# Kernel optimization log

Hardware: AMD Instinct MI355X
Metric: run time of the kernel (lower is better)

The kernel has to match this reference:

```python
import jax, jax.numpy as jnp
import numpy as np

H = 16          # num heads
HD = 64         # head dim
TEMPERATURE = 1.0
LN_EPS = 1e-5

def setup_inputs() -> dict:
    key = jax.random.key(0)
    ks = jax.random.split(key, 5)
    B, S, D = 2, 2048, 1024
    s = 1.0 / np.sqrt(D)
    return {
        "x": jax.random.normal(ks[0], (B, S, D), jnp.float32),
        "Wq": jax.random.normal(ks[1], (D, D), jnp.float32) * s,
        "bq": jnp.zeros((D,), jnp.float32),
        "Wk": jax.random.normal(ks[2], (D, D), jnp.float32) * s,
        "bk": jnp.zeros((D,), jnp.float32),
        "Wv": jax.random.normal(ks[3], (D, D), jnp.float32) * s,
        "bv": jnp.zeros((D,), jnp.float32),
        "Wo": jax.random.normal(ks[4], (D, D), jnp.float32) * s,
        "bo": jnp.zeros((D,), jnp.float32),
        "ln_gamma": jnp.ones((D,), jnp.float32),
        "ln_beta": jnp.zeros((D,), jnp.float32),
    }

def reference(x, Wq, bq, Wk, bk, Wv, bv, Wo, bo, ln_gamma, ln_beta):
    B, S, D = x.shape
    # LayerNorm (pre-attention)
    mu = jnp.mean(x, axis=-1, keepdims=True)
    var = jnp.mean(jnp.square(x - mu), axis=-1, keepdims=True)
    xn = (x - mu) * jax.lax.rsqrt(var + LN_EPS) * ln_gamma + ln_beta
    # Fused QKV projections (equivalent to H per-head Linears concatenated)
    q = (xn @ Wq + bq).reshape(B, S, H, HD)
    k = (xn @ Wk + bk).reshape(B, S, H, HD)
    v = (xn @ Wv + bv).reshape(B, S, H, HD)
    scale = np.sqrt(HD) * TEMPERATURE
    scores = jnp.einsum("bqhd,bkhd->bhqk", q, k) / scale
    attn = jax.nn.softmax(scores, axis=-1)  # dropout p=0 -> identity
    ctx = jnp.einsum("bhqk,bkhd->bqhd", attn, v).reshape(B, S, D)
    out = ctx @ Wo + bo
    return x + out
```

## Files before the change

kernel.cpp:

```cpp
#include <hip/hip_runtime.h>
#include <hip/hip_bf16.h>

#define Bc   2
#define Sc   2048
#define Dc   1024
#define Hc   16
#define HDc  64
#define MR   (Bc * Sc)
#define TBK  32
#define LOG2E 1.44269504088896f

typedef __attribute__((ext_vector_type(8))) short bf16x8;
typedef __attribute__((ext_vector_type(4))) float f32x4;

__device__ __forceinline__ unsigned short f2bf(float f) {
    __hip_bfloat16 h = __float2bfloat16(f);
    return *reinterpret_cast<unsigned short*>(&h);
}

__device__ __forceinline__ void gll16(const unsigned short* g, unsigned short* l) {
    __builtin_amdgcn_global_load_lds(
        (__attribute__((address_space(1))) const unsigned int*)g,
        (__attribute__((address_space(3))) unsigned int*)l,
        16, 0, 0);
}

__global__ __launch_bounds__(256) void prep_kernel(
        const float* __restrict__ x, const float* __restrict__ gamma,
        const float* __restrict__ beta, unsigned short* __restrict__ xn,
        const float* __restrict__ W0, const float* __restrict__ W1,
        const float* __restrict__ W2, const float* __restrict__ W3,
        unsigned short* __restrict__ T0, unsigned short* __restrict__ T1,
        unsigned short* __restrict__ T2, unsigned short* __restrict__ T3) {
    __shared__ float tile[64][65];
    int idx = blockIdx.x;
    int t = threadIdx.x;

    if (idx < 1024) {
        int z = idx >> 8, rem = idx & 255;
        const float* W = (z == 0) ? W0 : (z == 1) ? W1 : (z == 2) ? W2 : W3;
        unsigned short* T = (z == 0) ? T0 : (z == 1) ? T1 : (z == 2) ? T2 : T3;
        int nb = (rem & 15) * 64, kb = (rem >> 4) * 64;
        int r0 = t >> 4, c4 = (t & 15) * 4;
        #pragma unroll
        for (int rr = 0; rr < 4; rr++) {
            int row = rr * 16 + r0;
            float4 v = *(const float4*)(W + (size_t)(kb + row) * Dc + nb + c4);
            tile[row][c4 + 0] = v.x; tile[row][c4 + 1] = v.y;
            tile[row][c4 + 2] = v.z; tile[row][c4 + 3] = v.w;
        }
        __syncthreads();
        #pragma unroll
        for (int rr = 0; rr < 4; rr++) {
            int nrow = rr * 16 + r0;
            ushort4 o;
            o.x = f2bf(tile[c4 + 0][nrow]); o.y = f2bf(tile[c4 + 1][nrow]);
            o.z = f2bf(tile[c4 + 2][nrow]); o.w = f2bf(tile[c4 + 3][nrow]);
            *(ushort4*)(T + (size_t)(nb + nrow) * Dc + kb + c4) = o;
        }
    } else {
        int row = idx - 1024;
        const float4* xr = (const float4*)(x + (size_t)row * Dc);
        float4 v = xr[t];
        float s  = v.x + v.y + v.z + v.w;
        float ss = v.x * v.x + v.y * v.y + v.z * v.z + v.w * v.w;
        #pragma unroll
        for (int off = 32; off; off >>= 1) {
            s  += __shfl_xor(s, off, 64);
            ss += __shfl_xor(ss, off, 64);
        }
        float* red = tile[0];
        int w = t >> 6, lane = t & 63;
        if (lane == 0) { red[w * 2] = s; red[w * 2 + 1] = ss; }
        __syncthreads();
        s  = red[0] + red[2] + red[4] + red[6];
        ss = red[1] + red[3] + red[5] + red[7];
        float mean = s * (1.0f / Dc);
        float var  = ss * (1.0f / Dc) - mean * mean;
        float rstd = rsqrtf(var + 1e-5f);
        float4 g = ((const float4*)gamma)[t], bb = ((const float4*)beta)[t];
        ushort4 o;
        o.x = f2bf((v.x - mean) * rstd * g.x + bb.x);
        o.y = f2bf((v.y - mean) * rstd * g.y + bb.y);
        o.z = f2bf((v.z - mean) * rstd * g.z + bb.z);
        o.w = f2bf((v.w - mean) * rstd * g.w + bb.w);
        *(ushort4*)(xn + (size_t)row * Dc + t * 4) = o;
    }
}

__device__ __forceinline__ void gemm_core(const unsigned short* __restrict__ A,
                                          const unsigned short* __restrict__ Wt,
                                          unsigned short* As, unsigned short* Bs,
                                          int m0, int n0, f32x4 acc[4][4]) {
    int t = threadIdx.x;
    int w = t >> 6, lane = t & 63;
    int l16 = lane & 15, quad = lane >> 4;
    int wm = (w >> 1) * 64, wn = (w & 1) * 64;

    int srow = lane >> 2;
    int scol = (lane & 3) * 8;
    const unsigned short* Ag = A  + (size_t)(m0 + w * 16 + srow) * Dc + scol;
    const unsigned short* Bg = Wt + (size_t)(n0 + w * 16 + srow) * Dc + scol;
    unsigned short* Asw = As + (w * 16) * TBK;
    unsigned short* Bsw = Bs + (w * 16) * TBK;

    for (int k0 = 0; k0 < Dc; k0 += TBK) {
        gll16(Ag + k0, Asw);
        gll16(Ag + k0 + (size_t)64 * Dc, Asw + 64 * TBK);
        gll16(Bg + k0, Bsw);
        gll16(Bg + k0 + (size_t)64 * Dc, Bsw + 64 * TBK);
        __syncthreads();
        bf16x8 af[4], bfr[4];
        #pragma unroll
        for (int i = 0; i < 4; i++) {
            af[i]  = *(const bf16x8*)(As + (wm + i * 16 + l16) * TBK + quad * 8);
            bfr[i] = *(const bf16x8*)(Bs + (wn + i * 16 + l16) * TBK + quad * 8);
        }
        #pragma unroll
        for (int i = 0; i < 4; i++)
            #pragma unroll
            for (int j = 0; j < 4; j++)
                acc[i][j] = __builtin_amdgcn_mfma_f32_16x16x32_bf16(af[i], bfr[j], acc[i][j], 0, 0, 0);
        __syncthreads();
    }
}

__global__ __launch_bounds__(256) void gemm_qkv_kernel(
        const unsigned short* __restrict__ A,
        const unsigned short* __restrict__ Wqt, const unsigned short* __restrict__ Wkt,
        const unsigned short* __restrict__ Wvt,
        const float* __restrict__ bq, const float* __restrict__ bk,
        const float* __restrict__ bv,
        unsigned short* __restrict__ Qb, unsigned short* __restrict__ Kb,
        unsigned short* __restrict__ Vtb) {
    __shared__ unsigned short As[128 * TBK];
    __shared__ unsigned short Bs[128 * TBK];
    int z = blockIdx.z;
    const unsigned short* Wt = (z == 0) ? Wqt : (z == 1) ? Wkt : Wvt;
    const float* bias = (z == 0) ? bq : (z == 1) ? bk : bv;
    unsigned short* Out = (z == 0) ? Qb : (z == 1) ? Kb : Vtb;
    float outscale = (z == 0) ? (0.125f * LOG2E) : 1.0f;

    int n0 = blockIdx.x * 128, m0 = blockIdx.y * 128;
    f32x4 acc[4][4];
    #pragma unroll
    for (int i = 0; i < 4; i++)
        #pragma unroll
        for (int j = 0; j < 4; j++) acc[i][j] = (f32x4){0.f, 0.f, 0.f, 0.f};

    gemm_core(A, Wt, As, Bs, m0, n0, acc);

    int t = threadIdx.x;
    int w = t >> 6, lane = t & 63;
    int l16 = lane & 15, quad = lane >> 4;
    int wm = (w >> 1) * 64, wn = (w & 1) * 64;
    int b = m0 >> 11;
    #pragma unroll
    for (int j = 0; j < 4; j++) {
        int col = n0 + wn + j * 16 + l16;
        float bb = bias[col];
        int h = col >> 6, d = col & 63;
        #pragma unroll
        for (int i = 0; i < 4; i++) {
            #pragma unroll
            for (int r = 0; r < 4; r++) {
                int row = m0 + wm + i * 16 + quad * 4 + r;
                int s = row & (Sc - 1);
                unsigned short v = f2bf((acc[i][j][r] + bb) * outscale);
                if (z != 2)
                    Out[(((size_t)(b * Hc + h)) * Sc + s) * HDc + d] = v;
                else
                    Out[(((size_t)(b * Hc + h)) * HDc + d) * Sc + s] = v;
            }
        }
    }
}

__global__ __launch_bounds__(256) void gemm_o_kernel(
        const unsigned short* __restrict__ A,
        const unsigned short* __restrict__ Wot,
        const float* __restrict__ bo, const float* __restrict__ resid,
        float* __restrict__ Out) {
    __shared__ unsigned short As[64 * TBK];
    __shared__ unsigned short Bs[128 * TBK];
    int t = threadIdx.x;
    int w = t >> 6, lane = t & 63;
    int l16 = lane & 15, quad = lane >> 4;
    int wm = (w >> 1) * 32, wn = (w & 1) * 64;
    int n0 = blockIdx.x * 128, m0 = blockIdx.y * 64;

    f32x4 acc[2][4];
    #pragma unroll
    for (int i = 0; i < 2; i++)
        #pragma unroll
        for (int j = 0; j < 4; j++) acc[i][j] = (f32x4){0.f, 0.f, 0.f, 0.f};

    int srow = lane >> 2;
    int scol = (lane & 3) * 8;
    const unsigned short* Ag = A   + (size_t)(m0 + w * 16 + srow) * Dc + scol;
    const unsigned short* Bg = Wot + (size_t)(n0 + w * 16 + srow) * Dc + scol;
    unsigned short* Asw = As + (w * 16) * TBK;
    unsigned short* Bsw = Bs + (w * 16) * TBK;

    for (int k0 = 0; k0 < Dc; k0 += TBK) {
        gll16(Ag + k0, Asw);
        gll16(Bg + k0, Bsw);
        gll16(Bg + k0 + (size_t)64 * Dc, Bsw + 64 * TBK);
        __syncthreads();
        bf16x8 af[2], bfr[4];
        #pragma unroll
        for (int i = 0; i < 2; i++)
            af[i]  = *(const bf16x8*)(As + (wm + i * 16 + l16) * TBK + quad * 8);
        #pragma unroll
        for (int j = 0; j < 4; j++)
            bfr[j] = *(const bf16x8*)(Bs + (wn + j * 16 + l16) * TBK + quad * 8);
        #pragma unroll
        for (int i = 0; i < 2; i++)
            #pragma unroll
            for (int j = 0; j < 4; j++)
                acc[i][j] = __builtin_amdgcn_mfma_f32_16x16x32_bf16(af[i], bfr[j], acc[i][j], 0, 0, 0);
        __syncthreads();
    }

    #pragma unroll
    for (int j = 0; j < 4; j++) {
        int col = n0 + wn + j * 16 + l16;
        float bb = bo[col];
        #pragma unroll
        for (int i = 0; i < 2; i++) {
            #pragma unroll
            for (int r = 0; r < 4; r++) {
                int row = m0 + wm + i * 16 + quad * 4 + r;
                size_t off = (size_t)row * Dc + col;
                Out[off] = acc[i][j][r] + bb + resid[off];
            }
        }
    }
}

#define BKa 64

__global__ __launch_bounds__(256, 2) void attn_mfma_kernel(
        const unsigned short* __restrict__ Q,
        const unsigned short* __restrict__ K,
        const unsigned short* __restrict__ Vt,
        unsigned short* __restrict__ O) {
    __shared__ unsigned short Ks[BKa * 64];
    __shared__ unsigned short Vs[HDc * 64];
    __shared__ unsigned short Ps[4 * 32 * 64];

    int t = threadIdx.x;
    int w = t >> 6, lane = t & 63;
    int quad = lane >> 4, l16 = lane & 15;

    int bid = blockIdx.x + gridDim.x * blockIdx.y;
    int q0 = (bid >> 5) * 128;
    int bh = bid & 31;
    size_t qkbase = (size_t)bh * Sc * HDc;
    size_t vbase  = (size_t)bh * HDc * Sc;

    bf16x8 qf[2][2];
    #pragma unroll
    for (int jq = 0; jq < 2; jq++) {
        const unsigned short* qr = Q + qkbase
            + (size_t)(q0 + w * 32 + jq * 16 + l16) * HDc + quad * 8;
        qf[jq][0] = *(const bf16x8*)(qr);
        qf[jq][1] = *(const bf16x8*)(qr + 32);
    }

    f32x4 Oacc[2][4];
    #pragma unroll
    for (int jq = 0; jq < 2; jq++)
        #pragma unroll
        for (int n = 0; n < 4; n++) Oacc[jq][n] = (f32x4){0.f, 0.f, 0.f, 0.f};
    float lacc[2] = {0.f, 0.f};

    int srow = t >> 2, sseg = t & 3;
    const unsigned short* Kg = K + qkbase + (size_t)srow * HDc + sseg * 16;
    const unsigned short* Vg = Vt + vbase + (size_t)srow * Sc + sseg * 16;
    unsigned short* pw = Ps + w * 32 * 64;
    int rm_w = srow & 7;
    unsigned short* ksw0 = Ks + srow * 64 + ((2 * sseg)     ^ rm_w) * 8;
    unsigned short* ksw1 = Ks + srow * 64 + ((2 * sseg + 1) ^ rm_w) * 8;
    unsigned short* vsw0 = Vs + srow * 64 + ((2 * sseg)     ^ rm_w) * 8;
    unsigned short* vsw1 = Vs + srow * 64 + ((2 * sseg + 1) ^ rm_w) * 8;
    int rm = l16 & 7;
    const int NT = Sc / BKa;

    bf16x8 kv0 = *(const bf16x8*)(Kg);
    bf16x8 kv1 = *(const bf16x8*)(Kg + 8);
    bf16x8 vv0 = *(const bf16x8*)(Vg);
    bf16x8 vv1 = *(const bf16x8*)(Vg + 8);

    for (int kt = 0; kt < NT; kt++) {
        __syncthreads();
        *(bf16x8*)(ksw0) = kv0;
        *(bf16x8*)(ksw1) = kv1;
        *(bf16x8*)(vsw0) = vv0;
        *(bf16x8*)(vsw1) = vv1;
        __syncthreads();

        int ktn = (kt + 1 < NT) ? kt + 1 : kt;
        const unsigned short* kgn = Kg + (size_t)ktn * BKa * HDc;
        const unsigned short* vgn = Vg + ktn * BKa;
        kv0 = *(const bf16x8*)(kgn);
        kv1 = *(const bf16x8*)(kgn + 8);
        vv0 = *(const bf16x8*)(vgn);
        vv1 = *(const bf16x8*)(vgn + 8);

        f32x4 st[2][4];
        __builtin_amdgcn_s_setprio(1);
        #pragma unroll
        for (int m = 0; m < 4; m++) {
            const unsigned short* kr = Ks + (m * 16 + l16) * 64;
            bf16x8 kf0 = *(const bf16x8*)(kr + (quad       ^ rm) * 8);
            bf16x8 kf1 = *(const bf16x8*)(kr + ((quad + 4) ^ rm) * 8);
            #pragma unroll
            for (int jq = 0; jq < 2; jq++) {
                f32x4 s = (f32x4){0.f, 0.f, 0.f, 0.f};
                s = __builtin_amdgcn_mfma_f32_16x16x32_bf16(kf0, qf[jq][0], s, 0, 0, 0);
                s = __builtin_amdgcn_mfma_f32_16x16x32_bf16(kf1, qf[jq][1], s, 0, 0, 0);
                st[jq][m] = s;
            }
        }
        __builtin_amdgcn_s_setprio(0);

        #pragma unroll
        for (int jq = 0; jq < 2; jq++) {
            unsigned short* pr = pw + (jq * 16 + l16) * 64;
            #pragma unroll
            for (int m = 0; m < 4; m++) {
                float p0 = __builtin_amdgcn_exp2f(st[jq][m][0]);
                float p1 = __builtin_amdgcn_exp2f(st[jq][m][1]);
                float p2 = __builtin_amdgcn_exp2f(st[jq][m][2]);
                float p3 = __builtin_amdgcn_exp2f(st[jq][m][3]);
                lacc[jq] += (p0 + p1) + (p2 + p3);
                ushort4 pk;
                pk.x = f2bf(p0); pk.y = f2bf(p1); pk.z = f2bf(p2); pk.w = f2bf(p3);
                *(ushort4*)(pr + ((2 * m + (quad >> 1)) ^ rm) * 8 + (quad & 1) * 4) = pk;
            }
        }

        __builtin_amdgcn_s_setprio(1);
        #pragma unroll
        for (int kk = 0; kk < 2; kk++) {
            bf16x8 vf[4];
            #pragma unroll
            for (int n = 0; n < 4; n++)
                vf[n] = *(const bf16x8*)(Vs + (n * 16 + l16) * 64
                                         + ((4 * kk + quad) ^ rm) * 8);
            #pragma unroll
            for (int jq = 0; jq < 2; jq++) {
                bf16x8 pf = *(const bf16x8*)(pw + (jq * 16 + l16) * 64
                                             + ((4 * kk + quad) ^ rm) * 8);
                #pragma unroll
                for (int n = 0; n < 4; n++)
                    Oacc[jq][n] = __builtin_amdgcn_mfma_f32_16x16x32_bf16(pf, vf[n], Oacc[jq][n], 0, 0, 0);
            }
        }
        __builtin_amdgcn_s_setprio(0);
    }

    int b = bh >> 4, h = bh & 15;
    #pragma unroll
    for (int jq = 0; jq < 2; jq++) {
        lacc[jq] += __shfl_xor(lacc[jq], 16, 64);
        lacc[jq] += __shfl_xor(lacc[jq], 32, 64);
        #pragma unroll
        for (int i = 0; i < 4; i++) {
            float li = __shfl(lacc[jq], quad * 4 + i, 64);
            float rl = 1.0f / li;
            int q = q0 + w * 32 + jq * 16 + quad * 4 + i;
            #pragma unroll
            for (int n = 0; n < 4; n++) {
                O[((size_t)(b * Sc + q)) * Dc + h * HDc + n * 16 + l16] =
                    f2bf(Oacc[jq][n][i] * rl);
            }
        }
    }
}

extern "C" void kernel_launch(void* const* d_in, const int* in_sizes, int n_in,
                              void* d_out, int out_size, void* d_ws, size_t ws_size,
                              hipStream_t stream) {
    const float* x     = (const float*)d_in[0];
    const float* Wq    = (const float*)d_in[1];
    const float* bq    = (const float*)d_in[2];
    const float* Wk    = (const float*)d_in[3];
    const float* bk    = (const float*)d_in[4];
    const float* Wv    = (const float*)d_in[5];
    const float* bv    = (const float*)d_in[6];
    const float* Wo    = (const float*)d_in[7];
    const float* bo    = (const float*)d_in[8];
    const float* gamma = (const float*)d_in[9];
    const float* beta  = (const float*)d_in[10];
    float* out = (float*)d_out;

    unsigned short* us = (unsigned short*)d_ws;
    const size_t NE = (size_t)MR * Dc;
    const size_t WE = (size_t)Dc * Dc;
    unsigned short* xn  = us;
    unsigned short* Qb  = us + NE;
    unsigned short* Kb  = us + 2 * NE;
    unsigned short* Vtb = us + 3 * NE;
    unsigned short* ctx = us + 4 * NE;
    unsigned short* Wqt = us + 5 * NE;
    unsigned short* Wkt = Wqt + WE;
    unsigned short* Wvt = Wkt + WE;
    unsigned short* Wot = Wvt + WE;

    prep_kernel<<<1024 + MR, 256, 0, stream>>>(x, gamma, beta, xn,
                                               Wq, Wk, Wv, Wo,
                                               Wqt, Wkt, Wvt, Wot);

    dim3 qkvgrid(Dc / 128, MR / 128, 3);
    gemm_qkv_kernel<<<qkvgrid, 256, 0, stream>>>(xn, Wqt, Wkt, Wvt, bq, bk, bv,
                                                 Qb, Kb, Vtb);

    dim3 agrid(Sc / 128, Bc * Hc);
    attn_mfma_kernel<<<agrid, 256, 0, stream>>>(Qb, Kb, Vtb, ctx);

    dim3 ogrid(Dc / 128, MR / 64);
    gemm_o_kernel<<<ogrid, 256, 0, stream>>>(ctx, Wot, bo, x, out);
}
```

Before: 195.5 us.

## Keep K fragments and softmax probabilities in registers, bypassing LDS in attention

```diff
diff --git a/kernel.cpp b/kernel.cpp
--- a/kernel.cpp
+++ b/kernel.cpp
@@ -12,6 +12,7 @@
 
 typedef __attribute__((ext_vector_type(8))) short bf16x8;
 typedef __attribute__((ext_vector_type(4))) float f32x4;
+typedef __attribute__((ext_vector_type(4))) unsigned int u32x4;
 
 __device__ __forceinline__ unsigned short f2bf(float f) {
     __hip_bfloat16 h = __float2bfloat16(f);
@@ -245,9 +246,7 @@
         const unsigned short* __restrict__ K,
         const unsigned short* __restrict__ Vt,
         unsigned short* __restrict__ O) {
-    __shared__ unsigned short Ks[BKa * 64];
     __shared__ unsigned short Vs[HDc * 64];
-    __shared__ unsigned short Ps[4 * 32 * 64];
 
     int t = threadIdx.x;
     int w = t >> 6, lane = t & 63;
@@ -276,68 +275,84 @@
     float lacc[2] = {0.f, 0.f};
 
     int srow = t >> 2, sseg = t & 3;
-    const unsigned short* Kg = K + qkbase + (size_t)srow * HDc + sseg * 16;
     const unsigned short* Vg = Vt + vbase + (size_t)srow * Sc + sseg * 16;
-    unsigned short* pw = Ps + w * 32 * 64;
-    int rm_w = srow & 7;
-    unsigned short* ksw0 = Ks + srow * 64 + ((2 * sseg)     ^ rm_w) * 8;
-    unsigned short* ksw1 = Ks + srow * 64 + ((2 * sseg + 1) ^ rm_w) * 8;
-    unsigned short* vsw0 = Vs + srow * 64 + ((2 * sseg)     ^ rm_w) * 8;
-    unsigned short* vsw1 = Vs + srow * 64 + ((2 * sseg + 1) ^ rm_w) * 8;
+    int rk = srow & 7;
+    unsigned short* vsw0 = Vs + srow * 64 + ((2 * sseg)     ^ rk) * 8;
+    unsigned short* vsw1 = Vs + srow * 64 + ((2 * sseg + 1) ^ rk) * 8;
     int rm = l16 & 7;
     const int NT = Sc / BKa;
 
-    bf16x8 kv0 = *(const bf16x8*)(Kg);
-    bf16x8 kv1 = *(const bf16x8*)(Kg + 8);
+    const unsigned short* Kf = K + qkbase + (size_t)l16 * HDc + quad * 8;
+
     bf16x8 vv0 = *(const bf16x8*)(Vg);
     bf16x8 vv1 = *(const bf16x8*)(Vg + 8);
+    bf16x8 kf[4][2];
+    #pragma unroll
+    for (int m = 0; m < 4; m++) {
+        kf[m][0] = *(const bf16x8*)(Kf + (size_t)(m * 16) * HDc);
+        kf[m][1] = *(const bf16x8*)(Kf + (size_t)(m * 16) * HDc + 32);
+    }
 
     for (int kt = 0; kt < NT; kt++) {
         __syncthreads();
-        *(bf16x8*)(ksw0) = kv0;
-        *(bf16x8*)(ksw1) = kv1;
         *(bf16x8*)(vsw0) = vv0;
         *(bf16x8*)(vsw1) = vv1;
         __syncthreads();
 
         int ktn = (kt + 1 < NT) ? kt + 1 : kt;
-        const unsigned short* kgn = Kg + (size_t)ktn * BKa * HDc;
         const unsigned short* vgn = Vg + ktn * BKa;
-        kv0 = *(const bf16x8*)(kgn);
-        kv1 = *(const bf16x8*)(kgn + 8);
         vv0 = *(const bf16x8*)(vgn);
         vv1 = *(const bf16x8*)(vgn + 8);
+        bf16x8 kfn[4][2];
+        const unsigned short* kfb = Kf + (size_t)(ktn * BKa) * HDc;
+        #pragma unroll
+        for (int m = 0; m < 4; m++) {
+            kfn[m][0] = *(const bf16x8*)(kfb + (size_t)(m * 16) * HDc);
+            kfn[m][1] = *(const bf16x8*)(kfb + (size_t)(m * 16) * HDc + 32);
+        }
 
         f32x4 st[2][4];
         __builtin_amdgcn_s_setprio(1);
         #pragma unroll
         for (int m = 0; m < 4; m++) {
-            const unsigned short* kr = Ks + (m * 16 + l16) * 64;
-            bf16x8 kf0 = *(const bf16x8*)(kr + (quad       ^ rm) * 8);
-            bf16x8 kf1 = *(const bf16x8*)(kr + ((quad + 4) ^ rm) * 8);
             #pragma unroll
             for (int jq = 0; jq < 2; jq++) {
                 f32x4 s = (f32x4){0.f, 0.f, 0.f, 0.f};
-                s = __builtin_amdgcn_mfma_f32_16x16x32_bf16(kf0, qf[jq][0], s, 0, 0, 0);
-                s = __builtin_amdgcn_mfma_f32_16x16x32_bf16(kf1, qf[jq][1], s, 0, 0, 0);
+                s = __builtin_amdgcn_mfma_f32_16x16x32_bf16(kf[m][0], qf[jq][0], s, 0, 0, 0);
+                s = __builtin_amdgcn_mfma_f32_16x16x32_bf16(kf[m][1], qf[jq][1], s, 0, 0, 0);
                 st[jq][m] = s;
             }
         }
         __builtin_amdgcn_s_setprio(0);
 
+        u32x4 pa[2][2];
         #pragma unroll
         for (int jq = 0; jq < 2; jq++) {
-            unsigned short* pr = pw + (jq * 16 + l16) * 64;
+            float e[4][4];
             #pragma unroll
             for (int m = 0; m < 4; m++) {
-                float p0 = __builtin_amdgcn_exp2f(st[jq][m][0]);
-                float p1 = __builtin_amdgcn_exp2f(st[jq][m][1]);
-                float p2 = __builtin_amdgcn_exp2f(st[jq][m][2]);
-                float p3 = __builtin_amdgcn_exp2f(st[jq][m][3]);
-                lacc[jq] += (p0 + p1) + (p2 + p3);
-                ushort4 pk;
-                pk.x = f2bf(p0); pk.y = f2bf(p1); pk.z = f2bf(p2); pk.w = f2bf(p3);
-                *(ushort4*)(pr + ((2 * m + (quad >> 1)) ^ rm) * 8 + (quad & 1) * 4) = pk;
+                e[m][0] = __builtin_amdgcn_exp2f(st[jq][m][0]);
+                e[m][1] = __builtin_amdgcn_exp2f(st[jq][m][1]);
+                e[m][2] = __builtin_amdgcn_exp2f(st[jq][m][2]);
+                e[m][3] = __builtin_amdgcn_exp2f(st[jq][m][3]);
+                lacc[jq] += (e[m][0] + e[m][1]) + (e[m][2] + e[m][3]);
+            }
+            #pragma unroll
+            for (int kk = 0; kk < 2; kk++) {
+                unsigned int A, B, C, D;
+                asm("v_cvt_pk_bf16_f32 %0, %1, %2"
+                    : "=v"(A) : "v"(e[2 * kk][0]), "v"(e[2 * kk][1]));
+                asm("v_cvt_pk_bf16_f32 %0, %1, %2"
+                    : "=v"(B) : "v"(e[2 * kk][2]), "v"(e[2 * kk][3]));
+                asm("v_cvt_pk_bf16_f32 %0, %1, %2"
+                    : "=v"(C) : "v"(e[2 * kk + 1][0]), "v"(e[2 * kk + 1][1]));
+                asm("v_cvt_pk_bf16_f32 %0, %1, %2"
+                    : "=v"(D) : "v"(e[2 * kk + 1][2]), "v"(e[2 * kk + 1][3]));
+                asm("v_permlane32_swap_b32 %0, %1" : "+v"(A), "+v"(C));
+                asm("v_permlane32_swap_b32 %0, %1" : "+v"(B), "+v"(D));
+                asm("v_permlane16_swap_b32 %0, %1" : "+v"(A), "+v"(C));
+                asm("v_permlane16_swap_b32 %0, %1" : "+v"(B), "+v"(D));
+                pa[jq][kk] = (u32x4){A, B, C, D};
             }
         }
 
@@ -351,14 +366,19 @@
                                          + ((4 * kk + quad) ^ rm) * 8);
             #pragma unroll
             for (int jq = 0; jq < 2; jq++) {
-                bf16x8 pf = *(const bf16x8*)(pw + (jq * 16 + l16) * 64
-                                             + ((4 * kk + quad) ^ rm) * 8);
+                bf16x8 pf = *reinterpret_cast<const bf16x8*>(&pa[jq][kk]);
                 #pragma unroll
                 for (int n = 0; n < 4; n++)
                     Oacc[jq][n] = __builtin_amdgcn_mfma_f32_16x16x32_bf16(pf, vf[n], Oacc[jq][n], 0, 0, 0);
             }
         }
         __builtin_amdgcn_s_setprio(0);
+
+        #pragma unroll
+        for (int m = 0; m < 4; m++) {
+            kf[m][0] = kfn[m][0];
+            kf[m][1] = kfn[m][1];
+        }
     }
 
     int b = bh >> 4, h = bh & 15;
```

Result: slower. 217.4 us (+11.2%).
